# Kernel optimization log

Hardware: AMD Instinct MI355X
Metric: run time of the kernel (lower is better)

Reference implementation:

```python
import jax, jax.numpy as jnp
import numpy as np

N_NODES = 50000
N_EDGES = 1600000
IN_FEATS = 128
HIDDEN = 128
N_CLASSES = 16
N_GRAPHS = 512


def setup_inputs() -> dict:
    key = jax.random.key(0)
    ks = jax.random.split(key, 10)
    features = jax.random.normal(ks[0], (N_NODES, IN_FEATS), dtype=jnp.float32)
    src = jax.random.randint(ks[1], (N_EDGES,), 0, N_NODES, dtype=jnp.int32)
    dst = jax.random.randint(ks[2], (N_EDGES,), 0, N_NODES, dtype=jnp.int32)
    graph_ids = jnp.sort(jax.random.randint(ks[3], (N_NODES,), 0, N_GRAPHS, dtype=jnp.int32))
    # GraphConv weights (glorot-ish scaling) and biases
    W1 = jax.random.normal(ks[4], (IN_FEATS, HIDDEN), dtype=jnp.float32) / np.sqrt(IN_FEATS)
    b1 = jnp.zeros((HIDDEN,), dtype=jnp.float32)
    W2 = jax.random.normal(ks[5], (HIDDEN, HIDDEN), dtype=jnp.float32) / np.sqrt(HIDDEN)
    b2 = jnp.zeros((HIDDEN,), dtype=jnp.float32)
    Wf = jax.random.normal(ks[6], (HIDDEN, N_CLASSES), dtype=jnp.float32) / np.sqrt(HIDDEN)
    bf = jnp.zeros((N_CLASSES,), dtype=jnp.float32)
    return {"features": features, "W1": W1, "b1": b1, "W2": W2, "b2": b2,
            "Wf": Wf, "bf": bf, "src": src, "dst": dst, "graph_ids": graph_ids}


def _graph_conv(h, W, b, src, dst, norm_out, norm_in):
    # DGL GraphConv, norm='both': h' = D_in^{-1/2} * A^T * (D_out^{-1/2} * h) @ W + b
    h = h * norm_out[:, None]              # [N, d] scale by src out-degree
    agg = jax.ops.segment_sum(h[src], dst, num_segments=N_NODES)  # gather-scatter SpMM
    agg = agg * norm_in[:, None]
    return agg @ W + b


def reference(features, W1, b1, W2, b2, Wf, bf, src, dst, graph_ids):
    ones_e = jnp.ones((N_EDGES,), dtype=features.dtype)
    deg_out = jax.ops.segment_sum(ones_e, src, num_segments=N_NODES)
    deg_in = jax.ops.segment_sum(ones_e, dst, num_segments=N_NODES)
    norm_out = jnp.where(deg_out > 0, jax.lax.rsqrt(jnp.maximum(deg_out, 1.0)), 0.0)
    norm_in = jnp.where(deg_in > 0, jax.lax.rsqrt(jnp.maximum(deg_in, 1.0)), 0.0)

    x = jax.nn.relu(_graph_conv(features, W1, b1, src, dst, norm_out, norm_in))
    x = jax.nn.relu(_graph_conv(x, W2, b2, src, dst, norm_out, norm_in))

    # mean_nodes: per-graph mean pooling over batched graph
    sums = jax.ops.segment_sum(x, graph_ids, num_segments=N_GRAPHS)   # [G, d]
    counts = jax.ops.segment_sum(jnp.ones((N_NODES,), dtype=x.dtype), graph_ids,
                                 num_segments=N_GRAPHS)
    pooled = sums / jnp.maximum(counts, 1.0)[:, None]
    return pooled @ Wf + bf
```

## Files before the change

### kernel.cpp

```cpp
#include <hip/hip_runtime.h>

#define N_NODES 50000
#define N_EDGES 1600000
#define FEATS 128
#define N_GRAPHS 512
#define N_CLASSES 16

#define NC 400
#define CE 4000
#define NB 391
#define SLAB 4608
#define CSLAB 5632
#define ZROW 50000
#define SRC_MID 25000

typedef __attribute__((ext_vector_type(8))) short bf16x8;
typedef __attribute__((ext_vector_type(4))) float f32x4;

__device__ inline unsigned bf16_rne_bits(float x) {
    unsigned u = __float_as_uint(x);
    return (u + 0x7FFFu + ((u >> 16) & 1u)) >> 16;
}
__device__ inline unsigned pack_bf16(float a, float b) {
    return (bf16_rne_bits(b) << 16) | bf16_rne_bits(a);
}
__device__ inline float bf16lo(unsigned u) { return __uint_as_float(u << 16); }
__device__ inline float bf16hi(unsigned u) { return __uint_as_float(u & 0xFFFF0000u); }

__global__ __launch_bounds__(256) void countrank_kernel(
        const int* __restrict__ src, const int* __restrict__ dst,
        unsigned* __restrict__ ranks, unsigned* __restrict__ cntD, unsigned* __restrict__ cntS,
        const float* __restrict__ W1, const float* __restrict__ W2,
        unsigned short* __restrict__ t1h, unsigned short* __restrict__ t1l,
        unsigned short* __restrict__ t2h, unsigned short* __restrict__ t2l,
        int* __restrict__ gboth) {
    __shared__ unsigned hD[NB], hS[NB];
    if (blockIdx.x >= NC) {
        int b = blockIdx.x - NC;
        if (b == 0) {
#pragma unroll
            for (int i = 0; i < 4; ++i) gboth[threadIdx.x + 256 * i] = 0;
        }
        const float* W = (b < 64) ? W1 : W2;
        unsigned short* th = (b < 64) ? t1h : t2h;
        unsigned short* tl = (b < 64) ? t1l : t2l;
        int idx = (b & 63) * 256 + threadIdx.x;
        int k = idx >> 7;
        int col = idx & 127;
        float w = W[idx];
        unsigned hb = bf16_rne_bits(w);
        float hf = __uint_as_float(hb << 16);
        unsigned lb = bf16_rne_bits(w - hf);
        th[col * 128 + k] = (unsigned short)hb;
        tl[col * 128 + k] = (unsigned short)lb;
        return;
    }
    for (int i = threadIdx.x; i < NB; i += 256) { hD[i] = 0; hS[i] = 0; }
    __syncthreads();
    int c = blockIdx.x;
    int lo = c * CE;
    for (int i = lo + threadIdx.x; i < lo + CE; i += 256) {
        int d = dst[i];
        int s = src[i];
        unsigned rD = atomicAdd(&hD[d >> 7], 1u);
        unsigned rS = atomicAdd(&hS[s >> 7], 1u);
        ranks[i] = rD | (rS << 16);
    }
    __syncthreads();
    for (int i = threadIdx.x; i < NB; i += 256) {
        cntD[c * NB + i] = hD[i];
        cntS[c * NB + i] = hS[i];
    }
}

__global__ __launch_bounds__(512) void colscan_kernel(
        unsigned* __restrict__ cntD, unsigned* __restrict__ cntS,
        unsigned* __restrict__ totD, unsigned* __restrict__ totS) {
    int bb = blockIdx.x;
    unsigned* cnt = (bb < NB) ? cntD : cntS;
    unsigned* tot = (bb < NB) ? totD : totS;
    int col = (bb < NB) ? bb : bb - NB;
    __shared__ unsigned buf[512];
    int t = threadIdx.x;
    unsigned v = (t < NC) ? cnt[t * NB + col] : 0;
    buf[t] = v;
    __syncthreads();
    for (int off = 1; off < 512; off <<= 1) {
        unsigned add = (t >= off) ? buf[t - off] : 0;
        __syncthreads();
        buf[t] += add;
        __syncthreads();
    }
    if (t < NC) cnt[t * NB + col] = buf[t] - v;
    if (t == NC - 1) tot[col] = buf[t];
}

__global__ __launch_bounds__(256) void scatter_kernel(
        const int* __restrict__ src, const int* __restrict__ dst,
        const unsigned* __restrict__ ranks,
        const unsigned* __restrict__ colbaseD, const unsigned* __restrict__ colbaseS,
        unsigned* __restrict__ arenaD, unsigned char* __restrict__ arenaS) {
    __shared__ unsigned cbD[NB], cbS[NB];
    int c = blockIdx.x;
    for (int i = threadIdx.x; i < NB; i += 256) {
        cbD[i] = colbaseD[c * NB + i];
        cbS[i] = colbaseS[c * NB + i];
    }
    __syncthreads();
    int lo = c * CE;
    for (int i = lo + threadIdx.x; i < lo + CE; i += 256) {
        int d = dst[i];
        int s = src[i];
        unsigned rr = ranks[i];
        unsigned posD = (unsigned)(d >> 7) * SLAB + cbD[d >> 7] + (rr & 0xFFFFu);
        arenaD[posD] = (unsigned)s | ((unsigned)(d & 127) << 16);
        unsigned posS = (unsigned)(s >> 7) * SLAB + cbS[s >> 7] + (rr >> 16);
        arenaS[posS] = (unsigned char)(s & 127);
    }
}

__global__ __launch_bounds__(256) void finalize_kernel(
        const unsigned* __restrict__ arenaD, const unsigned* __restrict__ totD,
        const unsigned char* __restrict__ arenaS, const unsigned* __restrict__ totS,
        unsigned short* __restrict__ csr, unsigned* __restrict__ row_start,
        unsigned* __restrict__ cnt2,
        const float* __restrict__ X, unsigned* __restrict__ Xs,
        float* __restrict__ norm_in_a, float* __restrict__ norm_out_a,
        const int* __restrict__ gids, int* __restrict__ gstart, int* __restrict__ gend) {
    int b = blockIdx.x;
    __shared__ unsigned hlo[128], hhi[128], clo[128], chi[128], loc[128], sbuf[128], degs[128];
    __shared__ unsigned short stag[CSLAB];
    int t = threadIdx.x;
    if (t < 128) { hlo[t] = 0; hhi[t] = 0; clo[t] = 0; chi[t] = 0; }
    for (int i = t; i < CSLAB; i += 256) stag[i] = (unsigned short)ZROW;
    __syncthreads();
    unsigned nbS = totS[b];
    const unsigned char* slabS = arenaS + (size_t)b * SLAB;
    for (unsigned i = t; i < nbS; i += 256) atomicAdd(&clo[slabS[i]], 1u);
    __syncthreads();
    if (t < 128) { degs[t] = clo[t]; clo[t] = 0; }
    __syncthreads();
    unsigned nb = totD[b];
    const unsigned* slab = arenaD + (size_t)b * SLAB;
    for (unsigned i = t; i < nb; i += 256) {
        unsigned e = slab[i];
        if ((e & 0xFFFFu) < SRC_MID) atomicAdd(&hlo[e >> 16], 1u);
        else atomicAdd(&hhi[e >> 16], 1u);
    }
    __syncthreads();
    unsigned myv = 0;
    if (t < 128) {
        myv = ((hlo[t] + 7u) & ~7u) + ((hhi[t] + 7u) & ~7u);
        sbuf[t] = myv;
    }
    __syncthreads();
    for (int off = 1; off < 128; off <<= 1) {
        unsigned add = 0;
        if (t < 128 && t >= off) add = sbuf[t - off];
        __syncthreads();
        if (t < 128) sbuf[t] += add;
        __syncthreads();
    }
    if (t < 128) {
        loc[t] = sbuf[t] - myv;
        int dd = b * 128 + t;
        if (dd < N_NODES) {
            cnt2[dd] = hlo[t] | (hhi[t] << 16);
            row_start[dd] = (unsigned)b * CSLAB + loc[t];
        }
    }
    __syncthreads();
    for (unsigned i = t; i < nb; i += 256) {
        unsigned e = slab[i];
        unsigned dl = e >> 16;
        unsigned s = e & 0xFFFFu;
        unsigned pos;
        if (s < SRC_MID) pos = loc[dl] + atomicAdd(&clo[dl], 1u);
        else pos = loc[dl] + ((hlo[dl] + 7u) & ~7u) + atomicAdd(&chi[dl], 1u);
        stag[pos] = (unsigned short)s;
    }
    __syncthreads();
    unsigned tot_aligned = sbuf[127];
    unsigned short* g = csr + (size_t)b * CSLAB;
    for (unsigned i = t; i < tot_aligned; i += 256) g[i] = stag[i];
    for (int task = t; task < 128 * 16; task += 256) {
        int nl = task >> 4;
        int c = task & 15;
        int node = b * 128 + nl;
        if (node < N_NODES) {
            unsigned d0 = degs[nl];
            float no = d0 > 0 ? rsqrtf((float)d0) : 0.f;
            float4 a0 = *reinterpret_cast<const float4*>(X + (size_t)node * FEATS + c * 8);
            float4 a1 = *reinterpret_cast<const float4*>(X + (size_t)node * FEATS + c * 8 + 4);
            uint4 p;
            p.x = pack_bf16(a0.x * no, a0.y * no);
            p.y = pack_bf16(a0.z * no, a0.w * no);
            p.z = pack_bf16(a1.x * no, a1.y * no);
            p.w = pack_bf16(a1.z * no, a1.w * no);
            *reinterpret_cast<uint4*>(Xs + (size_t)node * (FEATS / 2) + c * 4) = p;
        } else if (node == ZROW) {
            uint4 z = {0u, 0u, 0u, 0u};
            *reinterpret_cast<uint4*>(Xs + (size_t)node * (FEATS / 2) + c * 4) = z;
        }
    }
    if (t < 128) {
        int node = b * 128 + t;
        if (node < N_NODES) {
            unsigned d0 = degs[t];
            norm_out_a[node] = d0 > 0 ? rsqrtf((float)d0) : 0.f;
            unsigned d1 = hlo[t] + hhi[t];
            norm_in_a[node] = d1 > 0 ? rsqrtf((float)d1) : 0.f;
            int g2 = gids[node];
            if (node == 0 || gids[node - 1] != g2) gstart[g2] = node;
            if (node == N_NODES - 1 || gids[node + 1] != g2) gend[g2] = node + 1;
        }
    }
}

__global__ __launch_bounds__(256) void agg_kernel(const unsigned* __restrict__ Xs,
        const unsigned short* __restrict__ csr, const unsigned* __restrict__ row_start,
        const unsigned* __restrict__ cnt2, unsigned* __restrict__ out) {
    int b = blockIdx.x;
    int h = b & 1;
    int node = (b >> 1) * 8 + (threadIdx.x >> 5);
    if (node >= N_NODES) return;
    int lane = threadIdx.x & 31;
    unsigned c2 = cnt2[node];
    unsigned ntot = (((c2 & 0xFFFFu) + 7u) & ~7u) + (((c2 >> 16) + 7u) & ~7u);
    const unsigned short* row = csr + row_start[node];
    const unsigned base = h * 32 + lane;
    float alo = 0.f, ahi = 0.f;
#pragma unroll 2
    for (unsigned j = 0; j < ntot; j += 8) {
        uint4 iv = *reinterpret_cast<const uint4*>(row + j);
        unsigned s0 = iv.x & 0xFFFFu, s1 = iv.x >> 16;
        unsigned s2 = iv.y & 0xFFFFu, s3 = iv.y >> 16;
        unsigned s4 = iv.z & 0xFFFFu, s5 = iv.z >> 16;
        unsigned s6 = iv.w & 0xFFFFu, s7 = iv.w >> 16;
        unsigned g0 = Xs[(size_t)s0 * 64 + base];
        unsigned g1 = Xs[(size_t)s1 * 64 + base];
        unsigned g2 = Xs[(size_t)s2 * 64 + base];
        unsigned g3 = Xs[(size_t)s3 * 64 + base];
        unsigned g4 = Xs[(size_t)s4 * 64 + base];
        unsigned g5 = Xs[(size_t)s5 * 64 + base];
        unsigned g6 = Xs[(size_t)s6 * 64 + base];
        unsigned g7 = Xs[(size_t)s7 * 64 + base];
        alo += ((bf16lo(g0) + bf16lo(g1)) + (bf16lo(g2) + bf16lo(g3)))
             + ((bf16lo(g4) + bf16lo(g5)) + (bf16lo(g6) + bf16lo(g7)));
        ahi += ((bf16hi(g0) + bf16hi(g1)) + (bf16hi(g2) + bf16hi(g3)))
             + ((bf16hi(g4) + bf16hi(g5)) + (bf16hi(g6) + bf16hi(g7)));
    }
    out[(size_t)node * 64 + base] = pack_bf16(alo, ahi);
}

template <bool BF16_OUT>
__global__ __launch_bounds__(256) void gemm_kernel(
        const unsigned* __restrict__ A,
        const unsigned short* __restrict__ Wth, const unsigned short* __restrict__ Wtl,
        const float* __restrict__ bias, const float* __restrict__ norm_in,
        const float* __restrict__ post, float* __restrict__ out_f32,
        unsigned short* __restrict__ out_b16, int n_rows) {
    __shared__ unsigned sWh[128 * 68];
    __shared__ unsigned sWl[128 * 68];
    {
        const uint4* gh = reinterpret_cast<const uint4*>(Wth);
        const uint4* gl = reinterpret_cast<const uint4*>(Wtl);
        for (int i = threadIdx.x; i < 2048; i += 256) {
            int col = i >> 4, q = i & 15;
            *reinterpret_cast<uint4*>(sWh + col * 68 + q * 4) = gh[i];
            *reinterpret_cast<uint4*>(sWl + col * 68 + q * 4) = gl[i];
        }
    }
    __syncthreads();

    const int l = threadIdx.x & 63;
    const int w = threadIdx.x >> 6;
    const int rl = l & 15;
    const int kg = l >> 4;
    const int row0 = blockIdx.x * 64 + w * 16;

    int row_a = row0 + rl;
    if (row_a >= n_rows) row_a = n_rows - 1;
    const uint4* Arow = reinterpret_cast<const uint4*>(A + (size_t)row_a * 64);

    f32x4 acc[8];
#pragma unroll
    for (int ct = 0; ct < 8; ++ct) acc[ct] = (f32x4){0.f, 0.f, 0.f, 0.f};

#pragma unroll
    for (int s = 0; s < 4; ++s) {
        bf16x8 af = __builtin_bit_cast(bf16x8, Arow[4 * s + kg]);
#pragma unroll
        for (int ct = 0; ct < 8; ++ct) {
            int colb = ct * 16 + rl;
            bf16x8 bh = __builtin_bit_cast(bf16x8,
                *reinterpret_cast<const uint4*>(sWh + colb * 68 + 16 * s + 4 * kg));
            bf16x8 bl = __builtin_bit_cast(bf16x8,
                *reinterpret_cast<const uint4*>(sWl + colb * 68 + 16 * s + 4 * kg));
            acc[ct] = __builtin_amdgcn_mfma_f32_16x16x32_bf16(af, bl, acc[ct], 0, 0, 0);
            acc[ct] = __builtin_amdgcn_mfma_f32_16x16x32_bf16(af, bh, acc[ct], 0, 0, 0);
        }
    }

    const int rb = row0 + kg * 4;
    float ni[4], po[4];
#pragma unroll
    for (int j = 0; j < 4; ++j) {
        int r = rb + j;
        bool v = r < n_rows;
        ni[j] = v ? norm_in[r] : 0.f;
        po[j] = (BF16_OUT && v) ? post[r] : 1.f;
    }
#pragma unroll
    for (int ct = 0; ct < 8; ++ct) {
        int col = ct * 16 + rl;
        float bc = bias[col];
#pragma unroll
        for (int j = 0; j < 4; ++j) {
            int r = rb + j;
            if (r < n_rows) {
                float o = fmaxf(fmaf(acc[ct][j], ni[j], bc), 0.f);
                if (BF16_OUT)
                    out_b16[(size_t)r * 128 + col] = (unsigned short)bf16_rne_bits(o * po[j]);
                else
                    out_f32[(size_t)r * 128 + col] = o;
            }
        }
    }
}

__global__ __launch_bounds__(256) void pool_final_kernel(
        const float* __restrict__ H, const int* __restrict__ gstart,
        const int* __restrict__ gend, const float* __restrict__ Wf,
        const float* __restrict__ bf, float* __restrict__ out) {
    int g = blockIdx.x;
    int s = gstart[g];
    int e = gend[g];
    int f = threadIdx.x & 127;
    int h = threadIdx.x >> 7;
    float acc = 0.f;
    for (int r = s + h; r < e; r += 2) acc += H[(size_t)r * FEATS + f];
    __shared__ float tmp[256];
    __shared__ float pooled[FEATS];
    tmp[threadIdx.x] = acc;
    __syncthreads();
    if (threadIdx.x < FEATS) {
        float inv = 1.0f / fmaxf((float)(e - s), 1.0f);
        pooled[threadIdx.x] = (tmp[threadIdx.x] + tmp[threadIdx.x + 128]) * inv;
    }
    __syncthreads();
    if (threadIdx.x < N_CLASSES) {
        int c = threadIdx.x;
        float d = bf[c];
        for (int k = 0; k < FEATS; ++k) d = fmaf(pooled[k], Wf[k * N_CLASSES + c], d);
        out[g * N_CLASSES + c] = d;
    }
}

extern "C" void kernel_launch(void* const* d_in, const int* in_sizes, int n_in,
                              void* d_out, int out_size, void* d_ws, size_t ws_size,
                              hipStream_t stream) {
    const float* features = (const float*)d_in[0];
    const float* W1 = (const float*)d_in[1];
    const float* b1 = (const float*)d_in[2];
    const float* W2 = (const float*)d_in[3];
    const float* b2 = (const float*)d_in[4];
    const float* Wf = (const float*)d_in[5];
    const float* bf = (const float*)d_in[6];
    const int* src = (const int*)d_in[7];
    const int* dst = (const int*)d_in[8];
    const int* gids = (const int*)d_in[9];
    float* out = (float*)d_out;

    char* wp = (char*)d_ws;
    auto alloc = [&wp](size_t bytes) {
        char* p = wp;
        wp += (bytes + 255) & ~(size_t)255;
        return p;
    };
    unsigned* buf0u = (unsigned*)alloc(((size_t)N_NODES + 1) * 64 * 4);
    float* buf1 = (float*)alloc((size_t)N_NODES * FEATS * 4 + 256);
    unsigned* B16 = (unsigned*)buf1;
    unsigned short* B16s = (unsigned short*)buf1;
    float* norm_in_a = (float*)alloc(N_NODES * 4);
    float* norm_out_a = (float*)alloc(N_NODES * 4);
    unsigned* cnt2 = (unsigned*)alloc(N_NODES * 4);
    unsigned* row_start = (unsigned*)alloc(N_NODES * 4);
    int* gboth = (int*)alloc(2 * N_GRAPHS * 4);
    int* gstart = gboth;
    int* gend = gboth + N_GRAPHS;
    unsigned short* t1h = (unsigned short*)alloc(4 * 16384 * 2);
    unsigned short* t1l = t1h + 16384;
    unsigned short* t2h = t1l + 16384;
    unsigned short* t2l = t2h + 16384;
    unsigned* cntD = (unsigned*)alloc((size_t)NC * NB * 4);
    unsigned* cntS = (unsigned*)alloc((size_t)NC * NB * 4);
    unsigned* totD = (unsigned*)alloc(NB * 4);
    unsigned* totS = (unsigned*)alloc(NB * 4);
    unsigned* arenaD = (unsigned*)alloc((size_t)NB * SLAB * 4);
    unsigned* ranks = (unsigned*)alloc((size_t)N_EDGES * 4);
    unsigned short* csr = (unsigned short*)ranks;
    unsigned char* arenaS = (unsigned char*)alloc((size_t)NB * SLAB);

    countrank_kernel<<<NC + 128, 256, 0, stream>>>(src, dst, ranks, cntD, cntS,
                                                   W1, W2, t1h, t1l, t2h, t2l, gboth);
    colscan_kernel<<<2 * NB, 512, 0, stream>>>(cntD, cntS, totD, totS);
    scatter_kernel<<<NC, 256, 0, stream>>>(src, dst, ranks, cntD, cntS, arenaD, arenaS);
    finalize_kernel<<<NB, 256, 0, stream>>>(arenaD, totD, arenaS, totS,
                                            csr, row_start, cnt2,
                                            features, B16, norm_in_a, norm_out_a,
                                            gids, gstart, gend);

    const int agg_blocks = 2 * ((N_NODES + 7) / 8);
    const int gemm_blocks = (N_NODES + 63) / 64;

    agg_kernel<<<agg_blocks, 256, 0, stream>>>(B16, csr, row_start, cnt2, buf0u);
    gemm_kernel<true><<<gemm_blocks, 256, 0, stream>>>(
        buf0u, t1h, t1l, b1, norm_in_a, norm_out_a, nullptr, B16s, N_NODES);

    agg_kernel<<<agg_blocks, 256, 0, stream>>>(B16, csr, row_start, cnt2, buf0u);
    gemm_kernel<false><<<gemm_blocks, 256, 0, stream>>>(
        buf0u, t2h, t2l, b2, norm_in_a, nullptr, buf1, nullptr, N_NODES);

    pool_final_kernel<<<N_GRAPHS, 256, 0, stream>>>(buf1, gstart, gend, Wf, bf, out);
}
```

Before: 207.2 us.

## Bin nodes by degree for load-balanced aggregation and emit bf16 layer-2 output

The finalize kernel now groups the 128 nodes of each block into degree bins and writes a permutation that the aggregation kernel uses to map warps to nodes. Warps in the same block therefore get similar edge counts, which reduces divergence and tail imbalance. The second GEMM now writes bf16 instead of fp32, and the pooling kernel reads bf16, halving that store and reload traffic. The cost is an extra indirection load per warp, slightly less locality in output writes, and lower precision in the pooled sum inputs.

```diff
diff --git a/kernel.cpp b/kernel.cpp
--- a/kernel.cpp
+++ b/kernel.cpp
@@ -9,6 +9,7 @@
 #define NC 400
 #define CE 4000
 #define NB 391
+#define NPAD (NB * 128)
 #define SLAB 4608
 #define CSLAB 5632
 #define ZROW 50000
@@ -123,15 +124,17 @@
         const unsigned* __restrict__ arenaD, const unsigned* __restrict__ totD,
         const unsigned char* __restrict__ arenaS, const unsigned* __restrict__ totS,
         unsigned short* __restrict__ csr, unsigned* __restrict__ row_start,
-        unsigned* __restrict__ cnt2,
+        unsigned* __restrict__ cnt2, int* __restrict__ aperm,
         const float* __restrict__ X, unsigned* __restrict__ Xs,
         float* __restrict__ norm_in_a, float* __restrict__ norm_out_a,
         const int* __restrict__ gids, int* __restrict__ gstart, int* __restrict__ gend) {
     int b = blockIdx.x;
     __shared__ unsigned hlo[128], hhi[128], clo[128], chi[128], loc[128], sbuf[128], degs[128];
+    __shared__ unsigned bcnt[32], bstart[32];
     __shared__ unsigned short stag[CSLAB];
     int t = threadIdx.x;
     if (t < 128) { hlo[t] = 0; hhi[t] = 0; clo[t] = 0; chi[t] = 0; }
+    if (t >= 128 && t < 160) bcnt[t - 128] = 0;
     for (int i = t; i < CSLAB; i += 256) stag[i] = (unsigned short)ZROW;
     __syncthreads();
     unsigned nbS = totS[b];
@@ -215,14 +218,33 @@
             if (node == N_NODES - 1 || gids[node + 1] != g2) gend[g2] = node + 1;
         }
     }
+    unsigned mybin = 0;
+    if (t < 128) {
+        mybin = min(myv >> 3, 31u);
+        atomicAdd(&bcnt[mybin], 1u);
+    }
+    __syncthreads();
+    if (t == 0) {
+        unsigned run = 0;
+#pragma unroll
+        for (int i = 0; i < 32; ++i) { bstart[i] = run; run += bcnt[i]; }
+    }
+    __syncthreads();
+    if (t < 128) {
+        unsigned pos = atomicAdd(&bstart[mybin], 1u);
+        aperm[b * 128 + pos] = b * 128 + t;
+    }
 }
 
 __global__ __launch_bounds__(256) void agg_kernel(const unsigned* __restrict__ Xs,
         const unsigned short* __restrict__ csr, const unsigned* __restrict__ row_start,
-        const unsigned* __restrict__ cnt2, unsigned* __restrict__ out) {
+        const unsigned* __restrict__ cnt2, const int* __restrict__ aperm,
+        unsigned* __restrict__ out) {
     int b = blockIdx.x;
     int h = b & 1;
-    int node = (b >> 1) * 8 + (threadIdx.x >> 5);
+    int idx = (b >> 1) * 8 + (threadIdx.x >> 5);
+    if (idx >= NPAD) return;
+    int node = aperm[idx];
     if (node >= N_NODES) return;
     int lane = threadIdx.x & 31;
     unsigned c2 = cnt2[node];
@@ -253,13 +275,12 @@
     out[(size_t)node * 64 + base] = pack_bf16(alo, ahi);
 }
 
-template <bool BF16_OUT>
 __global__ __launch_bounds__(256) void gemm_kernel(
         const unsigned* __restrict__ A,
         const unsigned short* __restrict__ Wth, const unsigned short* __restrict__ Wtl,
         const float* __restrict__ bias, const float* __restrict__ norm_in,
-        const float* __restrict__ post, float* __restrict__ out_f32,
-        unsigned short* __restrict__ out_b16, int n_rows) {
+        const float* __restrict__ post, unsigned short* __restrict__ out_b16,
+        int n_rows) {
     __shared__ unsigned sWh[128 * 68];
     __shared__ unsigned sWl[128 * 68];
     {
@@ -309,7 +330,7 @@
         int r = rb + j;
         bool v = r < n_rows;
         ni[j] = v ? norm_in[r] : 0.f;
-        po[j] = (BF16_OUT && v) ? post[r] : 1.f;
+        po[j] = (v && post) ? post[r] : 1.f;
     }
 #pragma unroll
     for (int ct = 0; ct < 8; ++ct) {
@@ -320,17 +341,14 @@
             int r = rb + j;
             if (r < n_rows) {
                 float o = fmaxf(fmaf(acc[ct][j], ni[j], bc), 0.f);
-                if (BF16_OUT)
-                    out_b16[(size_t)r * 128 + col] = (unsigned short)bf16_rne_bits(o * po[j]);
-                else
-                    out_f32[(size_t)r * 128 + col] = o;
+                out_b16[(size_t)r * 128 + col] = (unsigned short)bf16_rne_bits(o * po[j]);
             }
         }
     }
 }
 
 __global__ __launch_bounds__(256) void pool_final_kernel(
-        const float* __restrict__ H, const int* __restrict__ gstart,
+        const unsigned short* __restrict__ H, const int* __restrict__ gstart,
         const int* __restrict__ gend, const float* __restrict__ Wf,
         const float* __restrict__ bf, float* __restrict__ out) {
     int g = blockIdx.x;
@@ -339,7 +357,8 @@
     int f = threadIdx.x & 127;
     int h = threadIdx.x >> 7;
     float acc = 0.f;
-    for (int r = s + h; r < e; r += 2) acc += H[(size_t)r * FEATS + f];
+    for (int r = s + h; r < e; r += 2)
+        acc += __uint_as_float((unsigned)H[(size_t)r * FEATS + f] << 16);
     __shared__ float tmp[256];
     __shared__ float pooled[FEATS];
     tmp[threadIdx.x] = acc;
@@ -386,6 +405,7 @@
     float* norm_out_a = (float*)alloc(N_NODES * 4);
     unsigned* cnt2 = (unsigned*)alloc(N_NODES * 4);
     unsigned* row_start = (unsigned*)alloc(N_NODES * 4);
+    int* aperm = (int*)alloc((size_t)NPAD * 4);
     int* gboth = (int*)alloc(2 * N_GRAPHS * 4);
     int* gstart = gboth;
     int* gend = gboth + N_GRAPHS;
@@ -407,20 +427,20 @@
     colscan_kernel<<<2 * NB, 512, 0, stream>>>(cntD, cntS, totD, totS);
     scatter_kernel<<<NC, 256, 0, stream>>>(src, dst, ranks, cntD, cntS, arenaD, arenaS);
     finalize_kernel<<<NB, 256, 0, stream>>>(arenaD, totD, arenaS, totS,
-                                            csr, row_start, cnt2,
+                                            csr, row_start, cnt2, aperm,
                                             features, B16, norm_in_a, norm_out_a,
                                             gids, gstart, gend);
 
-    const int agg_blocks = 2 * ((N_NODES + 7) / 8);
+    const int agg_blocks = 2 * (NPAD / 8);
     const int gemm_blocks = (N_NODES + 63) / 64;
 
-    agg_kernel<<<agg_blocks, 256, 0, stream>>>(B16, csr, row_start, cnt2, buf0u);
-    gemm_kernel<true><<<gemm_blocks, 256, 0, stream>>>(
-        buf0u, t1h, t1l, b1, norm_in_a, norm_out_a, nullptr, B16s, N_NODES);
-
-    agg_kernel<<<agg_blocks, 256, 0, stream>>>(B16, csr, row_start, cnt2, buf0u);
-    gemm_kernel<false><<<gemm_blocks, 256, 0, stream>>>(
-        buf0u, t2h, t2l, b2, norm_in_a, nullptr, buf1, nullptr, N_NODES);
-
-    pool_final_kernel<<<N_GRAPHS, 256, 0, stream>>>(buf1, gstart, gend, Wf, bf, out);
-}
+    agg_kernel<<<agg_blocks, 256, 0, stream>>>(B16, csr, row_start, cnt2, aperm, buf0u);
+    gemm_kernel<<<gemm_blocks, 256, 0, stream>>>(
+        buf0u, t1h, t1l, b1, norm_in_a, norm_out_a, B16s, N_NODES);
+
+    agg_kernel<<<agg_blocks, 256, 0, stream>>>(B16, csr, row_start, cnt2, aperm, buf0u);
+    gemm_kernel<<<gemm_blocks, 256, 0, stream>>>(
+        buf0u, t2h, t2l, b2, norm_in_a, nullptr, B16s, N_NODES);
+
+    pool_final_kernel<<<N_GRAPHS, 256, 0, stream>>>(B16s, gstart, gend, Wf, bf, out);
+}
```

Result: slower. 219.4 us (+5.9%).
